# Kernel tuning notes

Measured on AMD Instinct MI355X. Metric: run time of the kernel, lower is better.

The kernel has to match this reference:

```python
import jax, jax.numpy as jnp
import numpy as np

B, TP, TH = 128, 128, 64
V, E, H, O = 50000, 300, 512, 3


def _lstm(x, lens, Wih, Whh, bih, bhh):
    # PyTorch LSTM, batch_first, gate order i,f,g,o; masked like pack_padded_sequence
    Bn, T, _ = x.shape
    Hn = Whh.shape[1]
    mask = jnp.arange(T)[None, :] < lens[:, None]  # [B,T]
    def step(carry, xt_mt):
        h, c = carry
        xt, mt = xt_mt  # [B,E], [B,1]
        g = xt @ Wih.T + h @ Whh.T + bih + bhh
        i, f, gg, o = jnp.split(g, 4, axis=-1)
        c_new = jax.nn.sigmoid(f) * c + jax.nn.sigmoid(i) * jnp.tanh(gg)
        h_new = jax.nn.sigmoid(o) * jnp.tanh(c_new)
        return (jnp.where(mt, h_new, h), jnp.where(mt, c_new, c)), jnp.where(mt, h_new, 0.0)
    z = jnp.zeros((Bn, Hn), x.dtype)
    _, hs = jax.lax.scan(step, (z, z), (jnp.swapaxes(x, 0, 1), jnp.swapaxes(mask, 0, 1)[..., None]))
    return jnp.swapaxes(hs, 0, 1)  # [B,T,H]


def _cell(x, h, c, Wih, Whh, bih, bhh):
    g = x @ Wih.T + h @ Whh.T + bih + bhh
    i, f, gg, o = jnp.split(g, 4, axis=-1)
    c_new = jax.nn.sigmoid(f) * c + jax.nn.sigmoid(i) * jnp.tanh(gg)
    h_new = jax.nn.sigmoid(o) * jnp.tanh(c_new)
    return h_new, c_new


def setup_inputs() -> dict:
    key = jax.random.key(0)
    ks = jax.random.split(key, 24)
    def unif(k, shape, fan):
        s = 1.0 / np.sqrt(fan)
        return jax.random.uniform(k, shape, jnp.float32, -s, s)
    inp = {}
    inp["premise"] = jax.random.randint(ks[0], (B, TP), 0, V, jnp.int32)
    inp["premise_len"] = jnp.full((B,), TP, jnp.int32)
    inp["hypothesis"] = jax.random.randint(ks[1], (B, TH), 0, V, jnp.int32)
    inp["hypothesis_len"] = jnp.full((B,), TH, jnp.int32)
    inp["embed_table"] = jax.random.normal(ks[2], (V, E), jnp.float32) * 0.1
    inp["embed_table"] = inp["embed_table"].at[0].set(0.0)  # padding_idx=0
    # premise LSTM
    inp["Wih_p"] = unif(ks[3], (4 * H, E), H); inp["Whh_p"] = unif(ks[4], (4 * H, H), H)
    inp["bih_p"] = unif(ks[5], (4 * H,), H); inp["bhh_p"] = unif(ks[6], (4 * H,), H)
    # hypothesis LSTM
    inp["Wih_h"] = unif(ks[7], (4 * H, E), H); inp["Whh_h"] = unif(ks[8], (4 * H, H), H)
    inp["bih_h"] = unif(ks[9], (4 * H,), H); inp["bhh_h"] = unif(ks[10], (4 * H,), H)
    # match LSTMCell (input 2H)
    inp["Wih_m"] = unif(ks[11], (4 * H, 2 * H), H); inp["Whh_m"] = unif(ks[12], (4 * H, H), H)
    inp["bih_m"] = unif(ks[13], (4 * H,), H); inp["bhh_m"] = unif(ks[14], (4 * H,), H)
    # attention
    inp["w_e"] = jax.random.uniform(ks[15], (H,), jnp.float32, 0.0, 1.0)
    inp["W_s"] = unif(ks[16], (H, H), H)
    inp["W_t"] = unif(ks[17], (H, H), H)
    inp["W_m"] = unif(ks[18], (H, H), H)
    inp["W_fc"] = unif(ks[19], (O, H), H)
    inp["b_fc"] = unif(ks[20], (O,), H)
    return inp


def reference(premise, premise_len, hypothesis, hypothesis_len, embed_table,
              Wih_p, Whh_p, bih_p, bhh_p, Wih_h, Whh_h, bih_h, bhh_h,
              Wih_m, Whh_m, bih_m, bhh_m, w_e, W_s, W_t, W_m, W_fc, b_fc):
    Bn = premise.shape[0]
    Hn = Whh_m.shape[1]
    p_emb = embed_table[premise]      # [B,Tp,E]
    h_emb = embed_table[hypothesis]   # [B,Th,E]
    h_s = _lstm(p_emb, premise_len, Wih_p, Whh_p, bih_p, bhh_p)      # [B,Tp,H]
    h_t = _lstm(h_emb, hypothesis_len, Wih_h, Whh_h, bih_h, bhh_h)   # [B,Th,H]
    Ws = jnp.einsum('bth,gh->btg', h_s, W_s)  # precompute w_s(h_s) once

    def step(carry, htk):
        h_m, c_m = carry
        q = htk @ W_t.T + h_m @ W_m.T                    # [B,H]
        s = jnp.tanh(Ws + q[:, None, :])                 # [B,Tp,H]
        e = s @ w_e                                      # [B,Tp]
        alpha = jax.nn.softmax(e, axis=1)                # softmax over premise positions
        a = jnp.einsum('bt,bth->bh', alpha, h_s)
        m_k = jnp.concatenate([a, htk], axis=1)          # [B,2H]
        h_m2, c_m2 = _cell(m_k, h_m, c_m, Wih_m, Whh_m, bih_m, bhh_m)
        return (h_m2, c_m2), h_m2

    z = jnp.zeros((Bn, Hn), h_s.dtype)
    _, hm_all = jax.lax.scan(step, (z, z), jnp.swapaxes(h_t, 0, 1))  # [Th,B,H]
    hm_all = jnp.swapaxes(hm_all, 0, 1)                              # [B,Th,H]
    idx = (hypothesis_len - 1).astype(jnp.int32)[:, None, None]
    last = jnp.take_along_axis(hm_all, idx, axis=1)[:, 0, :]         # last hidden per example
    return last @ W_fc.T + b_fc
```

## Files before the change

kernel.cpp:

```cpp
#include <hip/hip_runtime.h>
#include <hip/hip_bf16.h>

constexpr int BB = 128;
constexpr int TPp = 128;
constexpr int THh = 64;
constexpr int HH = 512;

constexpr size_t OFF_HS     = 0;
constexpr size_t SZ_HS      = (size_t)16384 * 512;
constexpr size_t OFF_HT     = OFF_HS + SZ_HS;
constexpr size_t SZ_HT      = (size_t)8192 * 512;
constexpr size_t OFF_WSM    = OFF_HT + SZ_HT;
constexpr size_t SZ_WSM     = (size_t)16384 * 512;
constexpr size_t OFF_XG_P   = OFF_WSM;
constexpr size_t OFF_XG_H   = OFF_WSM + (size_t)16 * 128 * 128 * 16;
constexpr size_t OFF_WIHT_P = OFF_WSM + SZ_WSM;
constexpr size_t SZ_WIHT    = (size_t)304 * 2048;
constexpr size_t OFF_WIHT_H = OFF_WIHT_P + SZ_WIHT;
constexpr size_t OFF_WHHT_P = OFF_WIHT_H + SZ_WIHT;
constexpr size_t OFF_WHHT_H = OFF_WHHT_P + (size_t)512 * 2048;
constexpr size_t OFF_WHHM2  = OFF_WHHT_H + (size_t)512 * 2048;
constexpr size_t OFF_WIA    = OFF_WHHM2 + (size_t)1024 * 2048;
constexpr size_t OFF_WMT2   = OFF_WIA + (size_t)512 * 2048;
constexpr size_t OFF_WEF    = OFF_WMT2 + (size_t)1024 * 512;
constexpr size_t OFF_BM     = OFF_WEF + 512;
constexpr size_t OFF_HC_P   = OFF_BM + 2048;
constexpr size_t OFF_HC_H   = OFF_HC_P + 2 * (size_t)BB * HH;
constexpr size_t OFF_C_P    = OFF_HC_H + 2 * (size_t)BB * HH;
constexpr size_t OFF_C_H    = OFF_C_P + (size_t)BB * HH;
constexpr size_t OFF_Q      = OFF_C_H + (size_t)BB * HH;
constexpr size_t OFF_GH     = OFF_Q + (size_t)BB * HH;
constexpr size_t OFF_A      = OFF_GH + (size_t)BB * 2048;
constexpr size_t OFF_HM     = OFF_A + (size_t)BB * HH;
constexpr size_t OFF_CM     = OFF_HM + (size_t)BB * HH;
constexpr size_t OFF_LAST   = OFF_CM + (size_t)BB * HH;
constexpr size_t WS_FLOATS  = OFF_LAST + (size_t)BB * HH;

__device__ __forceinline__ float sigmf(float x) { return 1.0f / (1.0f + __expf(-x)); }
__device__ __forceinline__ float tanh_f(float x) {
  float e = __expf(-2.0f * fabsf(x));
  float r = (1.0f - e) / (1.0f + e);
  return copysignf(r, x);
}

__global__ void k_diag(float* out, float v) {
  int i = blockIdx.x * 64 + threadIdx.x;
  if (i < BB * 3) out[i] = v;
}

__global__ __launch_bounds__(256) void k_prep(float* ws,
    const float* Wih_p, const float* bih_p, const float* bhh_p,
    const float* Wih_h, const float* bih_h, const float* bhh_h,
    const float* Whh_p, const float* Whh_h,
    const float* Whh_m, const float* Wih_m, const float* bih_m, const float* bhh_m,
    const float* W_m, const float* W_t, const float* w_e) {
  size_t gid = (size_t)blockIdx.x * 256 + threadIdx.x;
  if (gid < SZ_WIHT) {
    int k = (int)(gid >> 11), r = (int)(gid & 2047);
    float v = (k < 300) ? Wih_p[(size_t)r * 300 + k]
            : (k == 303) ? (bih_p[r] + bhh_p[r]) : 0.f;
    ws[OFF_WIHT_P + gid] = v;
    return;
  }
  gid -= SZ_WIHT;
  if (gid < SZ_WIHT) {
    int k = (int)(gid >> 11), r = (int)(gid & 2047);
    float v = (k < 300) ? Wih_h[(size_t)r * 300 + k]
            : (k == 303) ? (bih_h[r] + bhh_h[r]) : 0.f;
    ws[OFF_WIHT_H + gid] = v;
    return;
  }
  gid -= SZ_WIHT;
  const size_t NT = (size_t)512 * 2048;
  if (gid < NT) {
    int li = (int)(gid >> 13);
    int rem = (int)(gid & 8191);
    int k = rem >> 4, c = rem & 15;
    int jj = c >> 2, g = c & 3;
    ws[OFF_WHHT_P + gid] = Whh_p[(size_t)(g * 512 + li * 4 + jj) * 512 + k];
    return;
  }
  gid -= NT;
  if (gid < NT) {
    int li = (int)(gid >> 13);
    int rem = (int)(gid & 8191);
    int k = rem >> 4, c = rem & 15;
    int jj = c >> 2, g = c & 3;
    ws[OFF_WHHT_H + gid] = Whh_h[(size_t)(g * 512 + li * 4 + jj) * 512 + k];
    return;
  }
  gid -= NT;
  if (gid < (size_t)1024 * 2048) {
    int k = (int)(gid >> 11), r = (int)(gid & 2047);
    ws[OFF_WHHM2 + gid] = (k < 512) ? Whh_m[(size_t)r * 512 + k]
                                    : Wih_m[(size_t)r * 1024 + k];
    return;
  }
  gid -= (size_t)1024 * 2048;
  if (gid < NT) {
    int k = (int)(gid >> 11), c = (int)(gid & 2047);
    int j = c >> 2, g = c & 3;
    ws[OFF_WIA + gid] = Wih_m[((size_t)g * 512 + j) * 1024 + k];
    return;
  }
  gid -= NT;
  if (gid < (size_t)1024 * 512) {
    int k = (int)(gid >> 9), r = (int)(gid & 511);
    ws[OFF_WMT2 + gid] = (k < 512) ? W_m[(size_t)r * 512 + k]
                                   : W_t[(size_t)r * 512 + (k - 512)];
    return;
  }
  gid -= (size_t)1024 * 512;
  if (gid < 512) { ws[OFF_WEF + gid] = w_e[gid]; return; }
  gid -= 512;
  if (gid < 2048) { ws[OFF_BM + gid] = bih_m[gid] + bhh_m[gid]; return; }
  gid -= 2048;
  if (gid < (size_t)393216) { ws[OFF_HC_P + gid] = 0.f; return; }
  gid -= 393216;
  if (gid < (size_t)131072) { ws[OFF_HM + gid] = 0.f; return; }
}

__global__ __launch_bounds__(256) void k_gemm(const float* __restrict__ A,
                                              const float* __restrict__ Bw, int ldb, int Kdim,
                                              int N, float* __restrict__ C, int ntilesN) {
  __shared__ float As[16][68];
  __shared__ float Bs[16][68];
  const int tid = threadIdx.x;
  const int bid = blockIdx.x;
  const int tm = bid / ntilesN, tn = bid % ntilesN;
  const int m0 = tm * 64, n0 = tn * 64;
  const int tx = tid & 15, ty = tid >> 4;
  const int srow = tid >> 2, skc = (tid & 3) * 4;
  float acc[4][4] = {};
  const float* arowf = A + (size_t)(m0 + srow) * Kdim;
  const float* brow = Bw + (size_t)(n0 + srow) * ldb;
  for (int k0 = 0; k0 < Kdim; k0 += 16) {
    float4 v = *(const float4*)(arowf + k0 + skc);
    As[skc + 0][srow] = v.x; As[skc + 1][srow] = v.y;
    As[skc + 2][srow] = v.z; As[skc + 3][srow] = v.w;
#pragma unroll
    for (int i = 0; i < 4; i++) Bs[skc + i][srow] = brow[k0 + skc + i];
    __syncthreads();
#pragma unroll
    for (int kk = 0; kk < 16; kk++) {
      float4 a4 = *(float4*)&As[kk][ty * 4];
      float4 b4 = *(float4*)&Bs[kk][tx * 4];
      acc[0][0] += a4.x * b4.x; acc[0][1] += a4.x * b4.y; acc[0][2] += a4.x * b4.z; acc[0][3] += a4.x * b4.w;
      acc[1][0] += a4.y * b4.x; acc[1][1] += a4.y * b4.y; acc[1][2] += a4.y * b4.z; acc[1][3] += a4.y * b4.w;
      acc[2][0] += a4.z * b4.x; acc[2][1] += a4.z * b4.y; acc[2][2] += a4.z * b4.z; acc[2][3] += a4.z * b4.w;
      acc[3][0] += a4.w * b4.x; acc[3][1] += a4.w * b4.y; acc[3][2] += a4.w * b4.z; acc[3][3] += a4.w * b4.w;
    }
    __syncthreads();
  }
  const int m = m0 + ty * 4, n = n0 + tx * 4;
#pragma unroll
  for (int i = 0; i < 4; i++) {
    float4 o = {acc[i][0], acc[i][1], acc[i][2], acc[i][3]};
    *(float4*)&C[(size_t)(m + i) * N + n] = o;
  }
}

__global__ __launch_bounds__(256) void k_xg(float* __restrict__ ws,
    const int* __restrict__ premise, const int* __restrict__ hyp,
    const float* __restrict__ emb, int c0) {
  __shared__ float As[16][68];
  __shared__ float Bs[16][68];
  __shared__ int tok_lds[64];
  const int tid = threadIdx.x;
  const int bid = blockIdx.x;
  const int seq = bid >> 10;
  const int u = bid & 1023;
  const int tm = u >> 5, tn = u & 31;
  const int m0 = tm * 64, n0 = tn * 64;
  const int T = seq ? THh : TPp;
  const int* toks = seq ? hyp : premise;
  const float* WX = ws + (seq ? OFF_WIHT_H : OFF_WIHT_P);
  float* xg = ws + (seq ? OFF_XG_H : OFF_XG_P);
  if (tid < 64) {
    int r = m0 + tid;
    int tl = r >> 7, b = r & 127;
    tok_lds[tid] = toks[(size_t)b * T + c0 + tl];
  }
  __syncthreads();
  const int tx = tid & 15, ty = tid >> 4;
  const int sr = tid & 63, sk0 = (tid >> 6) * 4;
  const int bky = tid >> 4, bkx = (tid & 15) * 4;
  float acc[4][4] = {};
  for (int k0 = 0; k0 < 304; k0 += 16) {
    int tok = tok_lds[sr];
#pragma unroll
    for (int i = 0; i < 4; i++) {
      int k = k0 + sk0 + i;
      float v = 0.f;
      if (k < 300) v = emb[(size_t)tok * 300 + k];
      else if (k == 303) v = 1.f;
      As[sk0 + i][sr] = v;
    }
    *(float4*)&Bs[bky][bkx] = *(const float4*)(WX + (size_t)(k0 + bky) * 2048 + n0 + bkx);
    __syncthreads();
#pragma unroll
    for (int kk = 0; kk < 16; kk++) {
      float4 a4 = *(float4*)&As[kk][ty * 4];
      float4 b4 = *(float4*)&Bs[kk][tx * 4];
      acc[0][0] += a4.x * b4.x; acc[0][1] += a4.x * b4.y; acc[0][2] += a4.x * b4.z; acc[0][3] += a4.x * b4.w;
      acc[1][0] += a4.y * b4.x; acc[1][1] += a4.y * b4.y; acc[1][2] += a4.y * b4.z; acc[1][3] += a4.y * b4.w;
      acc[2][0] += a4.z * b4.x; acc[2][1] += a4.z * b4.y; acc[2][2] += a4.z * b4.z; acc[2][3] += a4.z * b4.w;
      acc[3][0] += a4.w * b4.x; acc[3][1] += a4.w * b4.y; acc[3][2] += a4.w * b4.z; acc[3][3] += a4.w * b4.w;
    }
    __syncthreads();
  }
  const int cbase = n0 + tx * 4;
  const int g = cbase >> 9;
  const int li = (cbase & 511) >> 2;
#pragma unroll
  for (int i = 0; i < 4; i++) {
    int r = m0 + ty * 4 + i;
    int tl = r >> 7, b = r & 127;
    float* dst = xg + (((size_t)tl * 128 + li) * 128 + b) * 16 + g;
#pragma unroll
    for (int jj = 0; jj < 4; jj++) dst[jj * 4] = acc[i][jj];
  }
}

__global__ __launch_bounds__(256) void k_step(float* __restrict__ ws,
    const int* __restrict__ plen, const int* __restrict__ hlen, int t) {
  __shared__ float4 wlds4[2048];
  __shared__ float4 hbuf4[2048];
  const int tid = threadIdx.x;
  const int bid = blockIdx.x;
  const int seq = bid >> 7;
  const int li = bid & 127;
  const int T = seq ? THh : TPp;
  const int* lens = seq ? hlen : plen;
  const float* wstk = ws + (seq ? OFF_WHHT_H : OFF_WHHT_P) + (size_t)li * 8192;
  const float* xg = ws + (seq ? OFF_XG_H : OFF_XG_P) + ((size_t)(t & 15) * 128 + li) * 2048;
  float* hsout = ws + (seq ? OFF_HT : OFF_HS);
  float* hc = ws + (seq ? OFF_HC_H : OFF_HC_P);
  float* cst = ws + (seq ? OFF_C_H : OFF_C_P) + (size_t)li * 512;
  const float* hin = hc + (size_t)(t & 1) * (BB * HH);
  float* hout = hc + (size_t)((t + 1) & 1) * (BB * HH);

  {
    const float4* src = (const float4*)wstk;
#pragma unroll
    for (int j = 0; j < 8; j++) wlds4[tid + j * 256] = src[tid + j * 256];
  }
  const int bg = tid & 63, cg = tid >> 6;
  const int b0 = 2 * bg, b1 = 2 * bg + 1;
  const int sw = bg & 7;
  float4 acc0 = {0.f, 0.f, 0.f, 0.f}, acc1 = {0.f, 0.f, 0.f, 0.f};

  float4 pre[8];
#pragma unroll
  for (int j = 0; j < 8; j++) {
    int fi = tid + j * 256, b = fi >> 4, k4 = fi & 15;
    pre[j] = *(const float4*)(hin + (size_t)b * 512 + k4 * 4);
  }
  for (int kc = 0; kc < 512; kc += 64) {
    __syncthreads();
#pragma unroll
    for (int j = 0; j < 8; j++) {
      int fi = tid + j * 256, b = fi >> 4, k4 = fi & 15;
      hbuf4[b * 16 + (k4 ^ ((b >> 1) & 7))] = pre[j];
    }
    __syncthreads();
    if (kc + 64 < 512) {
#pragma unroll
      for (int j = 0; j < 8; j++) {
        int fi = tid + j * 256, b = fi >> 4, k4 = fi & 15;
        pre[j] = *(const float4*)(hin + (size_t)b * 512 + (kc + 64) + k4 * 4);
      }
    }
#pragma unroll
    for (int kk = 0; kk < 64; kk += 4) {
      int k4 = kk >> 2;
      float4 h0 = hbuf4[b0 * 16 + (k4 ^ sw)];
      float4 h1 = hbuf4[b1 * 16 + (k4 ^ sw)];
      float4 w0 = wlds4[(kc + kk + 0) * 4 + cg];
      float4 w1 = wlds4[(kc + kk + 1) * 4 + cg];
      float4 w2 = wlds4[(kc + kk + 2) * 4 + cg];
      float4 w3 = wlds4[(kc + kk + 3) * 4 + cg];
      acc0.x += h0.x * w0.x + h0.y * w1.x + h0.z * w2.x + h0.w * w3.x;
      acc0.y += h0.x * w0.y + h0.y * w1.y + h0.z * w2.y + h0.w * w3.y;
      acc0.z += h0.x * w0.z + h0.y * w1.z + h0.z * w2.z + h0.w * w3.z;
      acc0.w += h0.x * w0.w + h0.y * w1.w + h0.z * w2.w + h0.w * w3.w;
      acc1.x += h1.x * w0.x + h1.y * w1.x + h1.z * w2.x + h1.w * w3.x;
      acc1.y += h1.x * w0.y + h1.y * w1.y + h1.z * w2.y + h1.w * w3.y;
      acc1.z += h1.x * w0.z + h1.y * w1.z + h1.z * w2.z + h1.w * w3.z;
      acc1.w += h1.x * w0.w + h1.y * w1.w + h1.z * w2.w + h1.w * w3.w;
    }
  }
  const int j = li * 4 + cg;
  float4 x0 = *(const float4*)(xg + (size_t)b0 * 16 + cg * 4);
  float4 x1 = *(const float4*)(xg + (size_t)b1 * 16 + cg * 4);
  {
    float gi = acc0.x + x0.x, gf = acc0.y + x0.y, gg = acc0.z + x0.z, go = acc0.w + x0.w;
    float iv = sigmf(gi), fv = sigmf(gf), gv = tanh_f(gg), ov = sigmf(go);
    float cold = cst[b0 * 4 + cg];
    float cn = fv * cold + iv * gv;
    float hn = ov * tanh_f(cn);
    bool inr = t < lens[b0];
    float hp = hin[(size_t)b0 * 512 + j];
    if (inr) cst[b0 * 4 + cg] = cn;
    hsout[((size_t)b0 * T + t) * 512 + j] = inr ? hn : 0.f;
    hout[(size_t)b0 * 512 + j] = inr ? hn : hp;
  }
  {
    float gi = acc1.x + x1.x, gf = acc1.y + x1.y, gg = acc1.z + x1.z, go = acc1.w + x1.w;
    float iv = sigmf(gi), fv = sigmf(gf), gv = tanh_f(gg), ov = sigmf(go);
    float cold = cst[b1 * 4 + cg];
    float cn = fv * cold + iv * gv;
    float hn = ov * tanh_f(cn);
    bool inr = t < lens[b1];
    float hp = hin[(size_t)b1 * 512 + j];
    if (inr) cst[b1 * 4 + cg] = cn;
    hsout[((size_t)b1 * T + t) * 512 + j] = inr ? hn : 0.f;
    hout[(size_t)b1 * 512 + j] = inr ? hn : hp;
  }
}

__global__ __launch_bounds__(256) void k_p1(float* __restrict__ ws, int k) {
  __shared__ float lds_a[16 * 1024];
  const int tid = threadIdx.x;
  const int task = blockIdx.x;
  const float* hm = ws + OFF_HM;
  const float* ht = ws + OFF_HT;
  const bool isq = task < 64;
  int mt, nt, ldb2;
  const float* BT;
  if (isq) { mt = task >> 3; nt = task & 7; BT = ws + OFF_WMT2; ldb2 = 512; }
  else { int u = task - 64; mt = u >> 5; nt = u & 31; BT = ws + OFF_WHHM2; ldb2 = 2048; }
  for (int i = tid; i < 2048; i += 256) {
    int row = i >> 7, c4 = i & 127;
    ((float4*)lds_a)[row * 256 + c4] =
        ((const float4*)(hm + (size_t)(mt * 16 + row) * 512))[c4];
    ((float4*)lds_a)[row * 256 + 128 + c4] =
        ((const float4*)(ht + ((size_t)(mt * 16 + row) * THh + k) * 512))[c4];
  }
  __syncthreads();
  const int tx = tid & 15, my = tid >> 4;
  const int ncol = nt * 64 + tx * 4;
  float4 acc = {0.f, 0.f, 0.f, 0.f};
  for (int kk = 0; kk < 1024; kk += 4) {
    float4 av = *(float4*)&lds_a[my * 1024 + kk];
    const float* bp = BT + (size_t)kk * ldb2 + ncol;
    float4 bv0 = *(const float4*)(bp);
    float4 bv1 = *(const float4*)(bp + ldb2);
    float4 bv2 = *(const float4*)(bp + 2 * (size_t)ldb2);
    float4 bv3 = *(const float4*)(bp + 3 * (size_t)ldb2);
    acc.x += av.x * bv0.x + av.y * bv1.x + av.z * bv2.x + av.w * bv3.x;
    acc.y += av.x * bv0.y + av.y * bv1.y + av.z * bv2.y + av.w * bv3.y;
    acc.z += av.x * bv0.z + av.y * bv1.z + av.z * bv2.z + av.w * bv3.z;
    acc.w += av.x * bv0.w + av.y * bv1.w + av.z * bv2.w + av.w * bv3.w;
  }
  const int m = mt * 16 + my;
  if (isq) *(float4*)&ws[OFF_Q + (size_t)m * 512 + ncol] = acc;
  else *(float4*)&ws[OFF_GH + (size_t)m * 2048 + ncol] = acc;
}

__global__ __launch_bounds__(256) void k_p2(float* __restrict__ ws) {
  __shared__ float q_lds[512];
  __shared__ float we_lds[512];
  __shared__ float e_part[256];
  __shared__ float e_lds[128];
  __shared__ float alpha_lds[128];
  __shared__ float red_s[2];
  const int tid = threadIdx.x;
  const int b = blockIdx.x;
  const float* q = ws + OFF_Q;
  const float* Wsb = ws + OFF_WSM;
  const float* hs = ws + OFF_HS;
  const float* wef = ws + OFF_WEF;
  float* abuf = ws + OFF_A;

  for (int i = tid; i < 512; i += 256) {
    q_lds[i] = q[(size_t)b * 512 + i];
    we_lds[i] = wef[i];
  }
  __syncthreads();
  {
    int t2 = tid >> 1;
    int gbase = (tid & 1) * 256;
    const float* wsrow = Wsb + ((size_t)b * TPp + t2) * 512 + gbase;
    float s = 0.f;
    for (int ii = 0; ii < 256; ii += 4) {
      float4 wv = *(const float4*)(wsrow + ii);
      float4 qv = *(float4*)&q_lds[gbase + ii];
      float4 ev = *(float4*)&we_lds[gbase + ii];
      s += tanh_f(wv.x + qv.x) * ev.x + tanh_f(wv.y + qv.y) * ev.y +
           tanh_f(wv.z + qv.z) * ev.z + tanh_f(wv.w + qv.w) * ev.w;
    }
    e_part[tid] = s;
  }
  __syncthreads();
  if (tid < 128) e_lds[tid] = e_part[tid * 2] + e_part[tid * 2 + 1];
  __syncthreads();
  if (tid < 64) {
    float m = fmaxf(e_lds[tid], e_lds[tid + 64]);
    for (int off = 32; off > 0; off >>= 1) m = fmaxf(m, __shfl_down(m, off));
    if (tid == 0) red_s[0] = m;
  }
  __syncthreads();
  if (tid < 128) alpha_lds[tid] = __expf(e_lds[tid] - red_s[0]);
  __syncthreads();
  if (tid < 64) {
    float s = alpha_lds[tid] + alpha_lds[tid + 64];
    for (int off = 32; off > 0; off >>= 1) s += __shfl_down(s, off);
    if (tid == 0) red_s[1] = 1.f / s;
  }
  __syncthreads();
  {
    float inv = red_s[1];
    float a0 = 0.f, a1 = 0.f;
    const float* hsb = hs + (size_t)b * TPp * 512 + tid * 2;
    for (int t2 = 0; t2 < TPp; t2++) {
      float2 hv = *(const float2*)(hsb + (size_t)t2 * 512);
      float al = alpha_lds[t2];
      a0 += al * hv.x;
      a1 += al * hv.y;
    }
    abuf[(size_t)b * 512 + tid * 2] = a0 * inv;
    abuf[(size_t)b * 512 + tid * 2 + 1] = a1 * inv;
  }
}

__global__ __launch_bounds__(256) void k_p3(float* __restrict__ ws, const int* __restrict__ hlen, int k) {
  __shared__ float lds_p3[16 * 512];
  const int tid = threadIdx.x;
  const int w = blockIdx.x;
  const int mt3 = w >> 5, jt3 = w & 31;
  const int my3 = tid >> 4, tx3 = tid & 15;
  const int b3 = mt3 * 16 + my3, j3 = jt3 * 16 + tx3;
  const int jcol4 = j3 * 4;
  const float* abuf = ws + OFF_A;
  const float* gh = ws + OFF_GH;
  const float* wia = ws + OFF_WIA;
  const float* bm = ws + OFF_BM;
  float* hm = ws + OFF_HM;
  float* cm = ws + OFF_CM;
  float* last = ws + OFF_LAST;

  {
    const float4* s4 = (const float4*)(abuf + (size_t)mt3 * 16 * 512);
    float4* d4 = (float4*)lds_p3;
    for (int i = tid; i < 2048; i += 256) d4[i] = s4[i];
  }
  __syncthreads();
  float a0 = 0.f, a1 = 0.f, a2 = 0.f, a3 = 0.f;
  for (int kk = 0; kk < 512; kk += 4) {
    float4 av = *(float4*)&lds_p3[my3 * 512 + kk];
    const float* wp = wia + (size_t)kk * 2048 + jcol4;
    float4 w0 = *(const float4*)(wp);
    float4 w1 = *(const float4*)(wp + 2048);
    float4 w2 = *(const float4*)(wp + 4096);
    float4 w3 = *(const float4*)(wp + 6144);
    a0 += av.x * w0.x + av.y * w1.x + av.z * w2.x + av.w * w3.x;
    a1 += av.x * w0.y + av.y * w1.y + av.z * w2.y + av.w * w3.y;
    a2 += av.x * w0.z + av.y * w1.z + av.z * w2.z + av.w * w3.z;
    a3 += av.x * w0.w + av.y * w1.w + av.z * w2.w + av.w * w3.w;
  }
  float gm[4] = {a0, a1, a2, a3};
#pragma unroll
  for (int g = 0; g < 4; g++) {
    int colg = g * 512 + j3;
    gm[g] += gh[(size_t)b3 * 2048 + colg] + bm[colg];
  }
  float iv = sigmf(gm[0]), fv = sigmf(gm[1]), gv = tanh_f(gm[2]), ov = sigmf(gm[3]);
  float cold = cm[(size_t)b3 * 512 + j3];
  float cn = fv * cold + iv * gv;
  float hn = ov * tanh_f(cn);
  cm[(size_t)b3 * 512 + j3] = cn;
  hm[(size_t)b3 * 512 + j3] = hn;
  if (k == hlen[b3] - 1) last[(size_t)b3 * 512 + j3] = hn;
}

__global__ __launch_bounds__(256) void k_fc(const float* __restrict__ ws, const float* __restrict__ Wfc,
                                            const float* __restrict__ bfc, float* __restrict__ out) {
  int idx = blockIdx.x * 256 + threadIdx.x;
  if (idx >= BB * 3) return;
  int b = idx / 3, o = idx - b * 3;
  const float* lrow = ws + OFF_LAST + (size_t)b * 512;
  const float* wrow = Wfc + (size_t)o * 512;
  float acc = bfc[o];
  for (int h = 0; h < 512; h++) acc += lrow[h] * wrow[h];
  out[idx] = acc;
}

extern "C" void kernel_launch(void* const* d_in, const int* in_sizes, int n_in, void* d_out,
                              int out_size, void* d_ws, size_t ws_size, hipStream_t stream) {
  const int* premise = (const int*)d_in[0];
  const int* plen = (const int*)d_in[1];
  const int* hyp = (const int*)d_in[2];
  const int* hlen = (const int*)d_in[3];
  const float* emb = (const float*)d_in[4];
  const float* Wih_p = (const float*)d_in[5];
  const float* Whh_p = (const float*)d_in[6];
  const float* bih_p = (const float*)d_in[7];
  const float* bhh_p = (const float*)d_in[8];
  const float* Wih_h = (const float*)d_in[9];
  const float* Whh_h = (const float*)d_in[10];
  const float* bih_h = (const float*)d_in[11];
  const float* bhh_h = (const float*)d_in[12];
  const float* Wih_m = (const float*)d_in[13];
  const float* Whh_m = (const float*)d_in[14];
  const float* bih_m = (const float*)d_in[15];
  const float* bhh_m = (const float*)d_in[16];
  const float* w_e = (const float*)d_in[17];
  const float* W_s = (const float*)d_in[18];
  const float* W_t = (const float*)d_in[19];
  const float* W_m = (const float*)d_in[20];
  const float* W_fc = (const float*)d_in[21];
  const float* b_fc = (const float*)d_in[22];
  float* ws = (float*)d_ws;
  float* out = (float*)d_out;

  if (ws_size < WS_FLOATS * sizeof(float)) {
    float mb = (float)((double)ws_size / (1024.0 * 1024.0));
    k_diag<<<dim3(6), dim3(64), 0, stream>>>(out, mb);
    return;
  }

  {
    size_t total = 2 * SZ_WIHT + 2 * (size_t)512 * 2048 + (size_t)1024 * 2048 +
                   (size_t)512 * 2048 + (size_t)1024 * 512 + 512 + 2048 + 393216 + 131072;
    int nb = (int)((total + 255) / 256);
    k_prep<<<dim3(nb), dim3(256), 0, stream>>>(ws, Wih_p, bih_p, bhh_p, Wih_h, bih_h, bhh_h,
                                               Whh_p, Whh_h, Whh_m, Wih_m, bih_m, bhh_m,
                                               W_m, W_t, w_e);
  }
  for (int t = 0; t < TPp; t++) {
    if ((t & 15) == 0) {
      int nb = (t < THh) ? 2048 : 1024;
      k_xg<<<dim3(nb), dim3(256), 0, stream>>>(ws, premise, hyp, emb, t);
    }
    int ns = (t < THh) ? 256 : 128;
    k_step<<<dim3(ns), dim3(256), 0, stream>>>(ws, plen, hlen, t);
  }
  k_gemm<<<dim3(256 * 8), dim3(256), 0, stream>>>(ws + OFF_HS, W_s, 512, 512, 512,
                                                  ws + OFF_WSM, 8);
  for (int k = 0; k < THh; k++) {
    k_p1<<<dim3(320), dim3(256), 0, stream>>>(ws, k);
    k_p2<<<dim3(128), dim3(256), 0, stream>>>(ws);
    k_p3<<<dim3(256), dim3(256), 0, stream>>>(ws, hlen, k);
  }
  k_fc<<<dim3(2), dim3(256), 0, stream>>>(ws, W_fc, b_fc, out);
}
```

Measured before the change: 12.45 ms.

## Fuse per-timestep LSTM and match launches into persistent cooperative kernels with grid barriers

Replaces the per-timestep launch loops (k_xg+k_step for the encoders, k_p1/k_p2/k_p3 for the match LSTM) with two persistent cooperative kernels of 256 blocks. These synchronise through atomic-counter grid barriers held in the workspace. Cell state now stays in registers, and each block's weight slices (recurrent weights, and the concatenated W_m/W_t/Whh_m/Wih_m matrix) are kept resident in shared memory. The goal is to remove hundreds of kernel launches and the repeated reloading of weights. The risks are barrier spin overhead and deadlock if the 256 blocks are not all co-resident, and the fallback to a normal launch does not guarantee co-residency.

```diff
diff --git a/kernel.cpp b/kernel.cpp
--- a/kernel.cpp
+++ b/kernel.cpp
@@ -19,10 +19,9 @@
 constexpr size_t OFF_WIHT_H = OFF_WIHT_P + SZ_WIHT;
 constexpr size_t OFF_WHHT_P = OFF_WIHT_H + SZ_WIHT;
 constexpr size_t OFF_WHHT_H = OFF_WHHT_P + (size_t)512 * 2048;
-constexpr size_t OFF_WHHM2  = OFF_WHHT_H + (size_t)512 * 2048;
-constexpr size_t OFF_WIA    = OFF_WHHM2 + (size_t)1024 * 2048;
-constexpr size_t OFF_WMT2   = OFF_WIA + (size_t)512 * 2048;
-constexpr size_t OFF_WEF    = OFF_WMT2 + (size_t)1024 * 512;
+constexpr size_t OFF_WB1T   = OFF_WHHT_H + (size_t)512 * 2048;
+constexpr size_t OFF_WIA    = OFF_WB1T + (size_t)2560 * 1024;
+constexpr size_t OFF_WEF    = OFF_WIA + (size_t)512 * 2048;
 constexpr size_t OFF_BM     = OFF_WEF + 512;
 constexpr size_t OFF_HC_P   = OFF_BM + 2048;
 constexpr size_t OFF_HC_H   = OFF_HC_P + 2 * (size_t)BB * HH;
@@ -34,13 +33,27 @@
 constexpr size_t OFF_HM     = OFF_A + (size_t)BB * HH;
 constexpr size_t OFF_CM     = OFF_HM + (size_t)BB * HH;
 constexpr size_t OFF_LAST   = OFF_CM + (size_t)BB * HH;
-constexpr size_t WS_FLOATS  = OFF_LAST + (size_t)BB * HH;
+constexpr size_t OFF_CNT    = OFF_LAST + (size_t)BB * HH;
+constexpr size_t WS_FLOATS  = OFF_CNT + 512;
 
 __device__ __forceinline__ float sigmf(float x) { return 1.0f / (1.0f + __expf(-x)); }
 __device__ __forceinline__ float tanh_f(float x) {
   float e = __expf(-2.0f * fabsf(x));
   float r = (1.0f - e) / (1.0f + e);
   return copysignf(r, x);
+}
+
+__device__ __forceinline__ void gbar(float* ws, int idx) {
+  __syncthreads();
+  if (threadIdx.x == 0) {
+    unsigned* cnt = (unsigned*)(ws + OFF_CNT) + idx;
+    __threadfence();
+    __hip_atomic_fetch_add(cnt, 1u, __ATOMIC_RELAXED, __HIP_MEMORY_SCOPE_AGENT);
+    while (__hip_atomic_load(cnt, __ATOMIC_RELAXED, __HIP_MEMORY_SCOPE_AGENT) < 256u)
+      __builtin_amdgcn_s_sleep(2);
+    __threadfence();
+  }
+  __syncthreads();
 }
 
 __global__ void k_diag(float* out, float v) {
@@ -90,13 +103,21 @@
     return;
   }
   gid -= NT;
-  if (gid < (size_t)1024 * 2048) {
-    int k = (int)(gid >> 11), r = (int)(gid & 2047);
-    ws[OFF_WHHM2 + gid] = (k < 512) ? Whh_m[(size_t)r * 512 + k]
-                                    : Wih_m[(size_t)r * 1024 + k];
+  if (gid < (size_t)2560 * 1024) {
+    int c = (int)(gid >> 10), k = (int)(gid & 1023);
+    float v;
+    if (c < 512) {
+      v = (k < 512) ? W_m[(size_t)c * 512 + k] : W_t[(size_t)c * 512 + (k - 512)];
+    } else {
+      int p = c - 512;
+      int j = p >> 2, g = p & 3;
+      int r = g * 512 + j;
+      v = (k < 512) ? Whh_m[(size_t)r * 512 + k] : Wih_m[(size_t)r * 1024 + k];
+    }
+    ws[OFF_WB1T + gid] = v;
     return;
   }
-  gid -= (size_t)1024 * 2048;
+  gid -= (size_t)2560 * 1024;
   if (gid < NT) {
     int k = (int)(gid >> 11), c = (int)(gid & 2047);
     int j = c >> 2, g = c & 3;
@@ -104,13 +125,6 @@
     return;
   }
   gid -= NT;
-  if (gid < (size_t)1024 * 512) {
-    int k = (int)(gid >> 9), r = (int)(gid & 511);
-    ws[OFF_WMT2 + gid] = (k < 512) ? W_m[(size_t)r * 512 + k]
-                                   : W_t[(size_t)r * 512 + (k - 512)];
-    return;
-  }
-  gid -= (size_t)1024 * 512;
   if (gid < 512) { ws[OFF_WEF + gid] = w_e[gid]; return; }
   gid -= 512;
   if (gid < 2048) { ws[OFF_BM + gid] = bih_m[gid] + bhh_m[gid]; return; }
@@ -118,6 +132,8 @@
   if (gid < (size_t)393216) { ws[OFF_HC_P + gid] = 0.f; return; }
   gid -= 393216;
   if (gid < (size_t)131072) { ws[OFF_HM + gid] = 0.f; return; }
+  gid -= 131072;
+  if (gid < 512) { ws[OFF_CNT + gid] = 0.f; return; }
 }
 
 __global__ __launch_bounds__(256) void k_gemm(const float* __restrict__ A,
@@ -160,72 +176,17 @@
   }
 }
 
-__global__ __launch_bounds__(256) void k_xg(float* __restrict__ ws,
+__global__ __launch_bounds__(256) void k_lstm_mega(float* __restrict__ ws,
     const int* __restrict__ premise, const int* __restrict__ hyp,
-    const float* __restrict__ emb, int c0) {
-  __shared__ float As[16][68];
-  __shared__ float Bs[16][68];
-  __shared__ int tok_lds[64];
-  const int tid = threadIdx.x;
-  const int bid = blockIdx.x;
-  const int seq = bid >> 10;
-  const int u = bid & 1023;
-  const int tm = u >> 5, tn = u & 31;
-  const int m0 = tm * 64, n0 = tn * 64;
-  const int T = seq ? THh : TPp;
-  const int* toks = seq ? hyp : premise;
-  const float* WX = ws + (seq ? OFF_WIHT_H : OFF_WIHT_P);
-  float* xg = ws + (seq ? OFF_XG_H : OFF_XG_P);
-  if (tid < 64) {
-    int r = m0 + tid;
-    int tl = r >> 7, b = r & 127;
-    tok_lds[tid] = toks[(size_t)b * T + c0 + tl];
-  }
-  __syncthreads();
-  const int tx = tid & 15, ty = tid >> 4;
-  const int sr = tid & 63, sk0 = (tid >> 6) * 4;
-  const int bky = tid >> 4, bkx = (tid & 15) * 4;
-  float acc[4][4] = {};
-  for (int k0 = 0; k0 < 304; k0 += 16) {
-    int tok = tok_lds[sr];
-#pragma unroll
-    for (int i = 0; i < 4; i++) {
-      int k = k0 + sk0 + i;
-      float v = 0.f;
-      if (k < 300) v = emb[(size_t)tok * 300 + k];
-      else if (k == 303) v = 1.f;
-      As[sk0 + i][sr] = v;
-    }
-    *(float4*)&Bs[bky][bkx] = *(const float4*)(WX + (size_t)(k0 + bky) * 2048 + n0 + bkx);
-    __syncthreads();
-#pragma unroll
-    for (int kk = 0; kk < 16; kk++) {
-      float4 a4 = *(float4*)&As[kk][ty * 4];
-      float4 b4 = *(float4*)&Bs[kk][tx * 4];
-      acc[0][0] += a4.x * b4.x; acc[0][1] += a4.x * b4.y; acc[0][2] += a4.x * b4.z; acc[0][3] += a4.x * b4.w;
-      acc[1][0] += a4.y * b4.x; acc[1][1] += a4.y * b4.y; acc[1][2] += a4.y * b4.z; acc[1][3] += a4.y * b4.w;
-      acc[2][0] += a4.z * b4.x; acc[2][1] += a4.z * b4.y; acc[2][2] += a4.z * b4.z; acc[2][3] += a4.z * b4.w;
-      acc[3][0] += a4.w * b4.x; acc[3][1] += a4.w * b4.y; acc[3][2] += a4.w * b4.z; acc[3][3] += a4.w * b4.w;
-    }
-    __syncthreads();
-  }
-  const int cbase = n0 + tx * 4;
-  const int g = cbase >> 9;
-  const int li = (cbase & 511) >> 2;
-#pragma unroll
-  for (int i = 0; i < 4; i++) {
-    int r = m0 + ty * 4 + i;
-    int tl = r >> 7, b = r & 127;
-    float* dst = xg + (((size_t)tl * 128 + li) * 128 + b) * 16 + g;
-#pragma unroll
-    for (int jj = 0; jj < 4; jj++) dst[jj * 4] = acc[i][jj];
-  }
-}
-
-__global__ __launch_bounds__(256) void k_step(float* __restrict__ ws,
-    const int* __restrict__ plen, const int* __restrict__ hlen, int t) {
-  __shared__ float4 wlds4[2048];
-  __shared__ float4 hbuf4[2048];
+    const int* __restrict__ plen, const int* __restrict__ hlen,
+    const float* __restrict__ emb) {
+  __shared__ float4 smem4[4096];
+  float4* wlds4 = smem4;
+  float4* hbuf4 = smem4 + 2048;
+  float* xAs = (float*)(smem4 + 2048);
+  float* xBs = xAs + 16 * 68;
+  int* xTok = (int*)(xBs + 16 * 68);
+
   const int tid = threadIdx.x;
   const int bid = blockIdx.x;
   const int seq = bid >> 7;
@@ -233,245 +194,355 @@
   const int T = seq ? THh : TPp;
   const int* lens = seq ? hlen : plen;
   const float* wstk = ws + (seq ? OFF_WHHT_H : OFF_WHHT_P) + (size_t)li * 8192;
-  const float* xg = ws + (seq ? OFF_XG_H : OFF_XG_P) + ((size_t)(t & 15) * 128 + li) * 2048;
   float* hsout = ws + (seq ? OFF_HT : OFF_HS);
   float* hc = ws + (seq ? OFF_HC_H : OFF_HC_P);
-  float* cst = ws + (seq ? OFF_C_H : OFF_C_P) + (size_t)li * 512;
-  const float* hin = hc + (size_t)(t & 1) * (BB * HH);
-  float* hout = hc + (size_t)((t + 1) & 1) * (BB * HH);
 
   {
     const float4* src = (const float4*)wstk;
 #pragma unroll
-    for (int j = 0; j < 8; j++) wlds4[tid + j * 256] = src[tid + j * 256];
+    for (int j2 = 0; j2 < 8; j2++) wlds4[tid + j2 * 256] = src[tid + j2 * 256];
   }
   const int bg = tid & 63, cg = tid >> 6;
   const int b0 = 2 * bg, b1 = 2 * bg + 1;
   const int sw = bg & 7;
-  float4 acc0 = {0.f, 0.f, 0.f, 0.f}, acc1 = {0.f, 0.f, 0.f, 0.f};
-
-  float4 pre[8];
-#pragma unroll
-  for (int j = 0; j < 8; j++) {
-    int fi = tid + j * 256, b = fi >> 4, k4 = fi & 15;
-    pre[j] = *(const float4*)(hin + (size_t)b * 512 + k4 * 4);
-  }
-  for (int kc = 0; kc < 512; kc += 64) {
-    __syncthreads();
-#pragma unroll
-    for (int j = 0; j < 8; j++) {
-      int fi = tid + j * 256, b = fi >> 4, k4 = fi & 15;
-      hbuf4[b * 16 + (k4 ^ ((b >> 1) & 7))] = pre[j];
-    }
-    __syncthreads();
-    if (kc + 64 < 512) {
-#pragma unroll
-      for (int j = 0; j < 8; j++) {
-        int fi = tid + j * 256, b = fi >> 4, k4 = fi & 15;
-        pre[j] = *(const float4*)(hin + (size_t)b * 512 + (kc + 64) + k4 * 4);
-      }
-    }
-#pragma unroll
-    for (int kk = 0; kk < 64; kk += 4) {
-      int k4 = kk >> 2;
-      float4 h0 = hbuf4[b0 * 16 + (k4 ^ sw)];
-      float4 h1 = hbuf4[b1 * 16 + (k4 ^ sw)];
-      float4 w0 = wlds4[(kc + kk + 0) * 4 + cg];
-      float4 w1 = wlds4[(kc + kk + 1) * 4 + cg];
-      float4 w2 = wlds4[(kc + kk + 2) * 4 + cg];
-      float4 w3 = wlds4[(kc + kk + 3) * 4 + cg];
-      acc0.x += h0.x * w0.x + h0.y * w1.x + h0.z * w2.x + h0.w * w3.x;
-      acc0.y += h0.x * w0.y + h0.y * w1.y + h0.z * w2.y + h0.w * w3.y;
-      acc0.z += h0.x * w0.z + h0.y * w1.z + h0.z * w2.z + h0.w * w3.z;
-      acc0.w += h0.x * w0.w + h0.y * w1.w + h0.z * w2.w + h0.w * w3.w;
-      acc1.x += h1.x * w0.x + h1.y * w1.x + h1.z * w2.x + h1.w * w3.x;
-      acc1.y += h1.x * w0.y + h1.y * w1.y + h1.z * w2.y + h1.w * w3.y;
-      acc1.z += h1.x * w0.z + h1.y * w1.z + h1.z * w2.z + h1.w * w3.z;
-      acc1.w += h1.x * w0.w + h1.y * w1.w + h1.z * w2.w + h1.w * w3.w;
-    }
-  }
-  const int j = li * 4 + cg;
-  float4 x0 = *(const float4*)(xg + (size_t)b0 * 16 + cg * 4);
-  float4 x1 = *(const float4*)(xg + (size_t)b1 * 16 + cg * 4);
+  const int jcol = li * 4 + cg;
+  const int len0 = lens[b0], len1 = lens[b1];
+  float c0r = 0.f, c1r = 0.f, h0r = 0.f, h1r = 0.f;
+  int bi = 0;
+
+  for (int t = 0; t < TPp; t++) {
+    if ((t & 15) == 0) {
+      int ntl = (t < THh) ? 2048 : 1024;
+      __syncthreads();
+      for (int tile = bid; tile < ntl; tile += 256) {
+        const int seqx = tile >> 10;
+        const int u = tile & 1023;
+        const int tm = u >> 5, tn = u & 31;
+        const int m0 = tm * 64, n0 = tn * 64;
+        const int Tx = seqx ? THh : TPp;
+        const int* toks = seqx ? hyp : premise;
+        const float* WX = ws + (seqx ? OFF_WIHT_H : OFF_WIHT_P);
+        float* xg = ws + (seqx ? OFF_XG_H : OFF_XG_P);
+        if (tid < 64) {
+          int r = m0 + tid;
+          int tl = r >> 7, b = r & 127;
+          xTok[tid] = toks[(size_t)b * Tx + t + tl];
+        }
+        __syncthreads();
+        const int tx = tid & 15, ty = tid >> 4;
+        const int sr = tid & 63, sk0 = (tid >> 6) * 4;
+        const int bky = tid >> 4, bkx = (tid & 15) * 4;
+        float acc[4][4] = {};
+        for (int k0 = 0; k0 < 304; k0 += 16) {
+          int tok = xTok[sr];
+#pragma unroll
+          for (int i = 0; i < 4; i++) {
+            int kx = k0 + sk0 + i;
+            float v = 0.f;
+            if (kx < 300) v = emb[(size_t)tok * 300 + kx];
+            else if (kx == 303) v = 1.0f;
+            xAs[(sk0 + i) * 68 + sr] = v;
+          }
+          *(float4*)&xBs[bky * 68 + bkx] = *(const float4*)(WX + (size_t)(k0 + bky) * 2048 + n0 + bkx);
+          __syncthreads();
+#pragma unroll
+          for (int kk = 0; kk < 16; kk++) {
+            float4 a4 = *(float4*)&xAs[kk * 68 + ty * 4];
+            float4 b4 = *(float4*)&xBs[kk * 68 + tx * 4];
+            acc[0][0] += a4.x * b4.x; acc[0][1] += a4.x * b4.y; acc[0][2] += a4.x * b4.z; acc[0][3] += a4.x * b4.w;
+            acc[1][0] += a4.y * b4.x; acc[1][1] += a4.y * b4.y; acc[1][2] += a4.y * b4.z; acc[1][3] += a4.y * b4.w;
+            acc[2][0] += a4.z * b4.x; acc[2][1] += a4.z * b4.y; acc[2][2] += a4.z * b4.z; acc[2][3] += a4.z * b4.w;
+            acc[3][0] += a4.w * b4.x; acc[3][1] += a4.w * b4.y; acc[3][2] += a4.w * b4.z; acc[3][3] += a4.w * b4.w;
+          }
+          __syncthreads();
+        }
+        const int cbase = n0 + tx * 4;
+        const int g = cbase >> 9;
+        const int li2 = (cbase & 511) >> 2;
+#pragma unroll
+        for (int i = 0; i < 4; i++) {
+          int r = m0 + ty * 4 + i;
+          int tl = r >> 7, b = r & 127;
+          float* dst = xg + (((size_t)tl * 128 + li2) * 128 + b) * 16 + g;
+#pragma unroll
+          for (int jj = 0; jj < 4; jj++) dst[jj * 4] = acc[i][jj];
+        }
+      }
+      gbar(ws, bi);
+      bi++;
+    }
+    const int par = t & 1;
+    const bool active = !(seq && t >= THh);
+    if (active) {
+      const float* hin = hc + (size_t)par * (BB * HH);
+      float* hout = hc + (size_t)(par ^ 1) * (BB * HH);
+      const float* xgp = ws + (seq ? OFF_XG_H : OFF_XG_P) + ((size_t)(t & 15) * 128 + li) * 2048;
+      float4 acc0 = {0.f, 0.f, 0.f, 0.f}, acc1 = {0.f, 0.f, 0.f, 0.f};
+      float4 pre[8];
+#pragma unroll
+      for (int j2 = 0; j2 < 8; j2++) {
+        int fi = tid + j2 * 256, b = fi >> 4, k4 = fi & 15;
+        pre[j2] = *(const float4*)(hin + (size_t)b * 512 + k4 * 4);
+      }
+      for (int kc = 0; kc < 512; kc += 64) {
+        __syncthreads();
+#pragma unroll
+        for (int j2 = 0; j2 < 8; j2++) {
+          int fi = tid + j2 * 256, b = fi >> 4, k4 = fi & 15;
+          hbuf4[b * 16 + (k4 ^ ((b >> 1) & 7))] = pre[j2];
+        }
+        __syncthreads();
+        if (kc + 64 < 512) {
+#pragma unroll
+          for (int j2 = 0; j2 < 8; j2++) {
+            int fi = tid + j2 * 256, b = fi >> 4, k4 = fi & 15;
+            pre[j2] = *(const float4*)(hin + (size_t)b * 512 + (kc + 64) + k4 * 4);
+          }
+        }
+#pragma unroll
+        for (int kk = 0; kk < 64; kk += 4) {
+          int k4 = kk >> 2;
+          float4 h0 = hbuf4[b0 * 16 + (k4 ^ sw)];
+          float4 h1 = hbuf4[b1 * 16 + (k4 ^ sw)];
+          float4 w0 = wlds4[(kc + kk + 0) * 4 + cg];
+          float4 w1 = wlds4[(kc + kk + 1) * 4 + cg];
+          float4 w2 = wlds4[(kc + kk + 2) * 4 + cg];
+          float4 w3 = wlds4[(kc + kk + 3) * 4 + cg];
+          acc0.x += h0.x * w0.x + h0.y * w1.x + h0.z * w2.x + h0.w * w3.x;
+          acc0.y += h0.x * w0.y + h0.y * w1.y + h0.z * w2.y + h0.w * w3.y;
+          acc0.z += h0.x * w0.z + h0.y * w1.z + h0.z * w2.z + h0.w * w3.z;
+          acc0.w += h0.x * w0.w + h0.y * w1.w + h0.z * w2.w + h0.w * w3.w;
+          acc1.x += h1.x * w0.x + h1.y * w1.x + h1.z * w2.x + h1.w * w3.x;
+          acc1.y += h1.x * w0.y + h1.y * w1.y + h1.z * w2.y + h1.w * w3.y;
+          acc1.z += h1.x * w0.z + h1.y * w1.z + h1.z * w2.z + h1.w * w3.z;
+          acc1.w += h1.x * w0.w + h1.y * w1.w + h1.z * w2.w + h1.w * w3.w;
+        }
+      }
+      float4 x0 = *(const float4*)(xgp + (size_t)b0 * 16 + cg * 4);
+      float4 x1 = *(const float4*)(xgp + (size_t)b1 * 16 + cg * 4);
+      {
+        float iv = sigmf(acc0.x + x0.x), fv = sigmf(acc0.y + x0.y);
+        float gv = tanh_f(acc0.z + x0.z), ov = sigmf(acc0.w + x0.w);
+        float cn = fv * c0r + iv * gv;
+        float hn = ov * tanh_f(cn);
+        bool inr = t < len0;
+        if (inr) { c0r = cn; h0r = hn; }
+        hsout[((size_t)b0 * T + t) * 512 + jcol] = inr ? hn : 0.f;
+        hout[(size_t)b0 * 512 + jcol] = h0r;
+      }
+      {
+        float iv = sigmf(acc1.x + x1.x), fv = sigmf(acc1.y + x1.y);
+        float gv = tanh_f(acc1.z + x1.z), ov = sigmf(acc1.w + x1.w);
+        float cn = fv * c1r + iv * gv;
+        float hn = ov * tanh_f(cn);
+        bool inr = t < len1;
+        if (inr) { c1r = cn; h1r = hn; }
+        hsout[((size_t)b1 * T + t) * 512 + jcol] = inr ? hn : 0.f;
+        hout[(size_t)b1 * 512 + jcol] = h1r;
+      }
+    }
+    gbar(ws, bi);
+    bi++;
+  }
+}
+
+__global__ __launch_bounds__(256) void k_match_mega(float* __restrict__ ws,
+                                                    const int* __restrict__ hlen) {
+  __shared__ float smem[16384];
+  float* B1 = smem;
+  float* W3 = smem + 10240;
+  float* AL = smem + 14336;
+  float* q_lds = AL; float* we_lds = AL + 512; float* e_part = AL + 1024;
+  float* e_lds = AL + 1280; float* alpha_lds = AL + 1408; float* red_s = AL + 1536;
+
+  const int tid = threadIdx.x;
+  const int bid = blockIdx.x;
+  float* hm = ws + OFF_HM;
+  const float* ht = ws + OFF_HT;
+  float* qbuf = ws + OFF_Q;
+  float* ghp = ws + OFF_GH;
+  float* abuf = ws + OFF_A;
+  float* last = ws + OFF_LAST;
+
   {
-    float gi = acc0.x + x0.x, gf = acc0.y + x0.y, gg = acc0.z + x0.z, go = acc0.w + x0.w;
-    float iv = sigmf(gi), fv = sigmf(gf), gv = tanh_f(gg), ov = sigmf(go);
-    float cold = cst[b0 * 4 + cg];
-    float cn = fv * cold + iv * gv;
-    float hn = ov * tanh_f(cn);
-    bool inr = t < lens[b0];
-    float hp = hin[(size_t)b0 * 512 + j];
-    if (inr) cst[b0 * 4 + cg] = cn;
-    hsout[((size_t)b0 * T + t) * 512 + j] = inr ? hn : 0.f;
-    hout[(size_t)b0 * 512 + j] = inr ? hn : hp;
-  }
-  {
-    float gi = acc1.x + x1.x, gf = acc1.y + x1.y, gg = acc1.z + x1.z, go = acc1.w + x1.w;
-    float iv = sigmf(gi), fv = sigmf(gf), gv = tanh_f(gg), ov = sigmf(go);
-    float cold = cst[b1 * 4 + cg];
-    float cn = fv * cold + iv * gv;
-    float hn = ov * tanh_f(cn);
-    bool inr = t < lens[b1];
-    float hp = hin[(size_t)b1 * 512 + j];
-    if (inr) cst[b1 * 4 + cg] = cn;
-    hsout[((size_t)b1 * T + t) * 512 + j] = inr ? hn : 0.f;
-    hout[(size_t)b1 * 512 + j] = inr ? hn : hp;
-  }
-}
-
-__global__ __launch_bounds__(256) void k_p1(float* __restrict__ ws, int k) {
-  __shared__ float lds_a[16 * 1024];
-  const int tid = threadIdx.x;
-  const int task = blockIdx.x;
-  const float* hm = ws + OFF_HM;
-  const float* ht = ws + OFF_HT;
-  const bool isq = task < 64;
-  int mt, nt, ldb2;
-  const float* BT;
-  if (isq) { mt = task >> 3; nt = task & 7; BT = ws + OFF_WMT2; ldb2 = 512; }
-  else { int u = task - 64; mt = u >> 5; nt = u & 31; BT = ws + OFF_WHHM2; ldb2 = 2048; }
-  for (int i = tid; i < 2048; i += 256) {
-    int row = i >> 7, c4 = i & 127;
-    ((float4*)lds_a)[row * 256 + c4] =
-        ((const float4*)(hm + (size_t)(mt * 16 + row) * 512))[c4];
-    ((float4*)lds_a)[row * 256 + 128 + c4] =
-        ((const float4*)(ht + ((size_t)(mt * 16 + row) * THh + k) * 512))[c4];
-  }
+    const float* wb1t = ws + OFF_WB1T + (size_t)bid * 10 * 1024;
+    for (int i = tid; i < 10 * 1024; i += 256) {
+      int cc = i >> 10, kk2 = i & 1023;
+      B1[cc * 1024 + kk2] = wb1t[(size_t)cc * 1024 + kk2];
+    }
+    const float* wia = ws + OFF_WIA;
+    for (int i = tid; i < 8 * 512; i += 256) {
+      int cc = i >> 9, kk2 = i & 511;
+      W3[cc * 512 + kk2] = wia[(size_t)kk2 * 2048 + bid * 8 + cc];
+    }
+  }
+  const int r = tid >> 1, half = tid & 1;
+  const int jj = half;
+  const int j3 = bid * 2 + jj;
+  float c_reg = 0.f;
+  float bmp[4];
+#pragma unroll
+  for (int g = 0; g < 4; g++) bmp[g] = ws[OFF_BM + g * 512 + j3];
+  const int hl = hlen[r];
+  int bi = 200;
   __syncthreads();
-  const int tx = tid & 15, my = tid >> 4;
-  const int ncol = nt * 64 + tx * 4;
-  float4 acc = {0.f, 0.f, 0.f, 0.f};
-  for (int kk = 0; kk < 1024; kk += 4) {
-    float4 av = *(float4*)&lds_a[my * 1024 + kk];
-    const float* bp = BT + (size_t)kk * ldb2 + ncol;
-    float4 bv0 = *(const float4*)(bp);
-    float4 bv1 = *(const float4*)(bp + ldb2);
-    float4 bv2 = *(const float4*)(bp + 2 * (size_t)ldb2);
-    float4 bv3 = *(const float4*)(bp + 3 * (size_t)ldb2);
-    acc.x += av.x * bv0.x + av.y * bv1.x + av.z * bv2.x + av.w * bv3.x;
-    acc.y += av.x * bv0.y + av.y * bv1.y + av.z * bv2.y + av.w * bv3.y;
-    acc.z += av.x * bv0.z + av.y * bv1.z + av.z * bv2.z + av.w * bv3.z;
-    acc.w += av.x * bv0.w + av.y * bv1.w + av.z * bv2.w + av.w * bv3.w;
-  }
-  const int m = mt * 16 + my;
-  if (isq) *(float4*)&ws[OFF_Q + (size_t)m * 512 + ncol] = acc;
-  else *(float4*)&ws[OFF_GH + (size_t)m * 2048 + ncol] = acc;
-}
-
-__global__ __launch_bounds__(256) void k_p2(float* __restrict__ ws) {
-  __shared__ float q_lds[512];
-  __shared__ float we_lds[512];
-  __shared__ float e_part[256];
-  __shared__ float e_lds[128];
-  __shared__ float alpha_lds[128];
-  __shared__ float red_s[2];
-  const int tid = threadIdx.x;
-  const int b = blockIdx.x;
-  const float* q = ws + OFF_Q;
-  const float* Wsb = ws + OFF_WSM;
-  const float* hs = ws + OFF_HS;
-  const float* wef = ws + OFF_WEF;
-  float* abuf = ws + OFF_A;
-
-  for (int i = tid; i < 512; i += 256) {
-    q_lds[i] = q[(size_t)b * 512 + i];
-    we_lds[i] = wef[i];
-  }
-  __syncthreads();
-  {
-    int t2 = tid >> 1;
-    int gbase = (tid & 1) * 256;
-    const float* wsrow = Wsb + ((size_t)b * TPp + t2) * 512 + gbase;
-    float s = 0.f;
-    for (int ii = 0; ii < 256; ii += 4) {
-      float4 wv = *(const float4*)(wsrow + ii);
-      float4 qv = *(float4*)&q_lds[gbase + ii];
-      float4 ev = *(float4*)&we_lds[gbase + ii];
-      s += tanh_f(wv.x + qv.x) * ev.x + tanh_f(wv.y + qv.y) * ev.y +
-           tanh_f(wv.z + qv.z) * ev.z + tanh_f(wv.w + qv.w) * ev.w;
-    }
-    e_part[tid] = s;
-  }
-  __syncthreads();
-  if (tid < 128) e_lds[tid] = e_part[tid * 2] + e_part[tid * 2 + 1];
-  __syncthreads();
-  if (tid < 64) {
-    float m = fmaxf(e_lds[tid], e_lds[tid + 64]);
-    for (int off = 32; off > 0; off >>= 1) m = fmaxf(m, __shfl_down(m, off));
-    if (tid == 0) red_s[0] = m;
-  }
-  __syncthreads();
-  if (tid < 128) alpha_lds[tid] = __expf(e_lds[tid] - red_s[0]);
-  __syncthreads();
-  if (tid < 64) {
-    float s = alpha_lds[tid] + alpha_lds[tid + 64];
-    for (int off = 32; off > 0; off >>= 1) s += __shfl_down(s, off);
-    if (tid == 0) red_s[1] = 1.f / s;
-  }
-  __syncthreads();
-  {
-    float inv = red_s[1];
-    float a0 = 0.f, a1 = 0.f;
-    const float* hsb = hs + (size_t)b * TPp * 512 + tid * 2;
-    for (int t2 = 0; t2 < TPp; t2++) {
-      float2 hv = *(const float2*)(hsb + (size_t)t2 * 512);
-      float al = alpha_lds[t2];
-      a0 += al * hv.x;
-      a1 += al * hv.y;
-    }
-    abuf[(size_t)b * 512 + tid * 2] = a0 * inv;
-    abuf[(size_t)b * 512 + tid * 2 + 1] = a1 * inv;
-  }
-}
-
-__global__ __launch_bounds__(256) void k_p3(float* __restrict__ ws, const int* __restrict__ hlen, int k) {
-  __shared__ float lds_p3[16 * 512];
-  const int tid = threadIdx.x;
-  const int w = blockIdx.x;
-  const int mt3 = w >> 5, jt3 = w & 31;
-  const int my3 = tid >> 4, tx3 = tid & 15;
-  const int b3 = mt3 * 16 + my3, j3 = jt3 * 16 + tx3;
-  const int jcol4 = j3 * 4;
-  const float* abuf = ws + OFF_A;
-  const float* gh = ws + OFF_GH;
-  const float* wia = ws + OFF_WIA;
-  const float* bm = ws + OFF_BM;
-  float* hm = ws + OFF_HM;
-  float* cm = ws + OFF_CM;
-  float* last = ws + OFF_LAST;
-
-  {
-    const float4* s4 = (const float4*)(abuf + (size_t)mt3 * 16 * 512);
-    float4* d4 = (float4*)lds_p3;
-    for (int i = tid; i < 2048; i += 256) d4[i] = s4[i];
-  }
-  __syncthreads();
-  float a0 = 0.f, a1 = 0.f, a2 = 0.f, a3 = 0.f;
-  for (int kk = 0; kk < 512; kk += 4) {
-    float4 av = *(float4*)&lds_p3[my3 * 512 + kk];
-    const float* wp = wia + (size_t)kk * 2048 + jcol4;
-    float4 w0 = *(const float4*)(wp);
-    float4 w1 = *(const float4*)(wp + 2048);
-    float4 w2 = *(const float4*)(wp + 4096);
-    float4 w3 = *(const float4*)(wp + 6144);
-    a0 += av.x * w0.x + av.y * w1.x + av.z * w2.x + av.w * w3.x;
-    a1 += av.x * w0.y + av.y * w1.y + av.z * w2.y + av.w * w3.y;
-    a2 += av.x * w0.z + av.y * w1.z + av.z * w2.z + av.w * w3.z;
-    a3 += av.x * w0.w + av.y * w1.w + av.z * w2.w + av.w * w3.w;
-  }
-  float gm[4] = {a0, a1, a2, a3};
-#pragma unroll
-  for (int g = 0; g < 4; g++) {
-    int colg = g * 512 + j3;
-    gm[g] += gh[(size_t)b3 * 2048 + colg] + bm[colg];
-  }
-  float iv = sigmf(gm[0]), fv = sigmf(gm[1]), gv = tanh_f(gm[2]), ov = sigmf(gm[3]);
-  float cold = cm[(size_t)b3 * 512 + j3];
-  float cn = fv * cold + iv * gv;
-  float hn = ov * tanh_f(cn);
-  cm[(size_t)b3 * 512 + j3] = cn;
-  hm[(size_t)b3 * 512 + j3] = hn;
-  if (k == hlen[b3] - 1) last[(size_t)b3 * 512 + j3] = hn;
+
+  for (int k = 0; k < THh; k++) {
+    {
+      float acc1[5] = {0.f, 0.f, 0.f, 0.f, 0.f};
+      const int f0 = tid, f1 = tid + 256;
+      const int b0s = f0 >> 2, q40 = f0 & 3;
+      const int b1s = f1 >> 2, q41 = f1 & 3;
+      float4 p0 = *(const float4*)&hm[(size_t)b0s * 512 + q40 * 4];
+      float4 p1 = *(const float4*)&hm[(size_t)b1s * 512 + q41 * 4];
+      for (int kc = 0; kc < 1024; kc += 16) {
+        __syncthreads();
+        AL[(q40 * 4 + 0) * 128 + b0s] = p0.x;
+        AL[(q40 * 4 + 1) * 128 + b0s] = p0.y;
+        AL[(q40 * 4 + 2) * 128 + b0s] = p0.z;
+        AL[(q40 * 4 + 3) * 128 + b0s] = p0.w;
+        AL[(q41 * 4 + 0) * 128 + b1s] = p1.x;
+        AL[(q41 * 4 + 1) * 128 + b1s] = p1.y;
+        AL[(q41 * 4 + 2) * 128 + b1s] = p1.z;
+        AL[(q41 * 4 + 3) * 128 + b1s] = p1.w;
+        __syncthreads();
+        int kn = kc + 16;
+        if (kn < 1024) {
+          int k0a = kn + q40 * 4, k1a = kn + q41 * 4;
+          p0 = (k0a < 512) ? *(const float4*)&hm[(size_t)b0s * 512 + k0a]
+                           : *(const float4*)&ht[((size_t)b0s * THh + k) * 512 + (k0a - 512)];
+          p1 = (k1a < 512) ? *(const float4*)&hm[(size_t)b1s * 512 + k1a]
+                           : *(const float4*)&ht[((size_t)b1s * THh + k) * 512 + (k1a - 512)];
+        }
+        const int cb = half * 5;
+#pragma unroll
+        for (int kk = 0; kk < 16; kk += 4) {
+          float a0 = AL[(kk + 0) * 128 + r];
+          float a1 = AL[(kk + 1) * 128 + r];
+          float a2 = AL[(kk + 2) * 128 + r];
+          float a3 = AL[(kk + 3) * 128 + r];
+#pragma unroll
+          for (int cc = 0; cc < 5; cc++) {
+            float4 bv = *(float4*)&B1[(cb + cc) * 1024 + kc + kk];
+            acc1[cc] += a0 * bv.x + a1 * bv.y + a2 * bv.z + a3 * bv.w;
+          }
+        }
+      }
+      const int cbase = bid * 10 + half * 5;
+#pragma unroll
+      for (int cc = 0; cc < 5; cc++) {
+        int c = cbase + cc;
+        if (c < 512) qbuf[(size_t)r * 512 + c] = acc1[cc];
+        else ghp[(size_t)r * 2048 + (c - 512)] = acc1[cc];
+      }
+    }
+    gbar(ws, bi); bi++;
+    if (bid < 128) {
+      const int b = bid;
+      const float* Wsb = ws + OFF_WSM;
+      const float* hs = ws + OFF_HS;
+      const float* wef = ws + OFF_WEF;
+      for (int i = tid; i < 512; i += 256) {
+        q_lds[i] = qbuf[(size_t)b * 512 + i];
+        we_lds[i] = wef[i];
+      }
+      __syncthreads();
+      {
+        int t2 = tid >> 1;
+        int gbase = (tid & 1) * 256;
+        const float* wsrow = Wsb + ((size_t)b * TPp + t2) * 512 + gbase;
+        float s = 0.f;
+        for (int ii = 0; ii < 256; ii += 4) {
+          float4 wv = *(const float4*)(wsrow + ii);
+          float4 qv = *(float4*)&q_lds[gbase + ii];
+          float4 ev = *(float4*)&we_lds[gbase + ii];
+          s += tanh_f(wv.x + qv.x) * ev.x + tanh_f(wv.y + qv.y) * ev.y +
+               tanh_f(wv.z + qv.z) * ev.z + tanh_f(wv.w + qv.w) * ev.w;
+        }
+        e_part[tid] = s;
+      }
+      __syncthreads();
+      if (tid < 128) e_lds[tid] = e_part[tid * 2] + e_part[tid * 2 + 1];
+      __syncthreads();
+      if (tid < 64) {
+        float m = fmaxf(e_lds[tid], e_lds[tid + 64]);
+        for (int off = 32; off > 0; off >>= 1) m = fmaxf(m, __shfl_down(m, off));
+        if (tid == 0) red_s[0] = m;
+      }
+      __syncthreads();
+      if (tid < 128) alpha_lds[tid] = __expf(e_lds[tid] - red_s[0]);
+      __syncthreads();
+      if (tid < 64) {
+        float s = alpha_lds[tid] + alpha_lds[tid + 64];
+        for (int off = 32; off > 0; off >>= 1) s += __shfl_down(s, off);
+        if (tid == 0) red_s[1] = 1.f / s;
+      }
+      __syncthreads();
+      {
+        float inv = red_s[1];
+        float a0 = 0.f, a1 = 0.f;
+        const float* hsb = hs + (size_t)b * TPp * 512 + tid * 2;
+        for (int t2 = 0; t2 < TPp; t2++) {
+          float2 hv = *(const float2*)(hsb + (size_t)t2 * 512);
+          float al = alpha_lds[t2];
+          a0 += al * hv.x;
+          a1 += al * hv.y;
+        }
+        abuf[(size_t)b * 512 + tid * 2] = a0 * inv;
+        abuf[(size_t)b * 512 + tid * 2 + 1] = a1 * inv;
+      }
+    }
+    gbar(ws, bi); bi++;
+    {
+      float acc3[4] = {0.f, 0.f, 0.f, 0.f};
+      const int f0 = tid, f1 = tid + 256;
+      const int b0s = f0 >> 2, q40 = f0 & 3;
+      const int b1s = f1 >> 2, q41 = f1 & 3;
+      float4 p0 = *(const float4*)&abuf[(size_t)b0s * 512 + q40 * 4];
+      float4 p1 = *(const float4*)&abuf[(size_t)b1s * 512 + q41 * 4];
+      for (int kc = 0; kc < 512; kc += 16) {
+        __syncthreads();
+        AL[(q40 * 4 + 0) * 128 + b0s] = p0.x;
+        AL[(q40 * 4 + 1) * 128 + b0s] = p0.y;
+        AL[(q40 * 4 + 2) * 128 + b0s] = p0.z;
+        AL[(q40 * 4 + 3) * 128 + b0s] = p0.w;
+        AL[(q41 * 4 + 0) * 128 + b1s] = p1.x;
+        AL[(q41 * 4 + 1) * 128 + b1s] = p1.y;
+        AL[(q41 * 4 + 2) * 128 + b1s] = p1.z;
+        AL[(q41 * 4 + 3) * 128 + b1s] = p1.w;
+        __syncthreads();
+        int kn = kc + 16;
+        if (kn < 512) {
+          p0 = *(const float4*)&abuf[(size_t)b0s * 512 + kn + q40 * 4];
+          p1 = *(const float4*)&abuf[(size_t)b1s * 512 + kn + q41 * 4];
+        }
+#pragma unroll
+        for (int kk = 0; kk < 16; kk += 4) {
+          float a0 = AL[(kk + 0) * 128 + r];
+          float a1 = AL[(kk + 1) * 128 + r];
+          float a2 = AL[(kk + 2) * 128 + r];
+          float a3 = AL[(kk + 3) * 128 + r];
+#pragma unroll
+          for (int g = 0; g < 4; g++) {
+            float4 wv = *(float4*)&W3[(jj * 4 + g) * 512 + kc + kk];
+            acc3[g] += a0 * wv.x + a1 * wv.y + a2 * wv.z + a3 * wv.w;
+          }
+        }
+      }
+      float4 gh4 = *(const float4*)&ghp[(size_t)r * 2048 + j3 * 4];
+      float gi = acc3[0] + gh4.x + bmp[0];
+      float gf = acc3[1] + gh4.y + bmp[1];
+      float gg = acc3[2] + gh4.z + bmp[2];
+      float go = acc3[3] + gh4.w + bmp[3];
+      float iv = sigmf(gi), fv = sigmf(gf), gv = tanh_f(gg), ov = sigmf(go);
+      float cn = fv * c_reg + iv * gv;
+      float hn = ov * tanh_f(cn);
+      c_reg = cn;
+      hm[(size_t)r * 512 + j3] = hn;
+      if (k == hl - 1) last[(size_t)r * 512 + j3] = hn;
+    }
+    gbar(ws, bi); bi++;
+  }
 }
 
 __global__ __launch_bounds__(256) void k_fc(const float* __restrict__ ws, const float* __restrict__ Wfc,
@@ -521,27 +592,28 @@
   }
 
   {
-    size_t total = 2 * SZ_WIHT + 2 * (size_t)512 * 2048 + (size_t)1024 * 2048 +
-                   (size_t)512 * 2048 + (size_t)1024 * 512 + 512 + 2048 + 393216 + 131072;
+    size_t total = 2 * SZ_WIHT + 2 * (size_t)512 * 2048 + (size_t)2560 * 1024 +
+                   (size_t)512 * 2048 + 512 + 2048 + 393216 + 131072 + 512;
     int nb = (int)((total + 255) / 256);
     k_prep<<<dim3(nb), dim3(256), 0, stream>>>(ws, Wih_p, bih_p, bhh_p, Wih_h, bih_h, bhh_h,
                                                Whh_p, Whh_h, Whh_m, Wih_m, bih_m, bhh_m,
                                                W_m, W_t, w_e);
   }
-  for (int t = 0; t < TPp; t++) {
-    if ((t & 15) == 0) {
-      int nb = (t < THh) ? 2048 : 1024;
-      k_xg<<<dim3(nb), dim3(256), 0, stream>>>(ws, premise, hyp, emb, t);
-    }
-    int ns = (t < THh) ? 256 : 128;
-    k_step<<<dim3(ns), dim3(256), 0, stream>>>(ws, plen, hlen, t);
+  {
+    void* args[] = {(void*)&ws, (void*)&premise, (void*)&hyp, (void*)&plen, (void*)&hlen, (void*)&emb};
+    hipError_t e = hipLaunchCooperativeKernel((const void*)k_lstm_mega, dim3(256), dim3(256),
+                                              args, 0, stream);
+    if (e != hipSuccess)
+      k_lstm_mega<<<dim3(256), dim3(256), 0, stream>>>(ws, premise, hyp, plen, hlen, emb);
   }
   k_gemm<<<dim3(256 * 8), dim3(256), 0, stream>>>(ws + OFF_HS, W_s, 512, 512, 512,
                                                   ws + OFF_WSM, 8);
-  for (int k = 0; k < THh; k++) {
-    k_p1<<<dim3(320), dim3(256), 0, stream>>>(ws, k);
-    k_p2<<<dim3(128), dim3(256), 0, stream>>>(ws);
-    k_p3<<<dim3(256), dim3(256), 0, stream>>>(ws, hlen, k);
+  {
+    void* args[] = {(void*)&ws, (void*)&hlen};
+    hipError_t e = hipLaunchCooperativeKernel((const void*)k_match_mega, dim3(256), dim3(256),
+                                              args, 0, stream);
+    if (e != hipSuccess)
+      k_match_mega<<<dim3(256), dim3(256), 0, stream>>>(ws, hlen);
   }
   k_fc<<<dim3(2), dim3(256), 0, stream>>>(ws, W_fc, b_fc, out);
 }
```

After: 20.70 ms. 1.66x slower.
